# Kernel tuning notes

Measured on AMD Instinct MI355X. Metric: run time of the kernel, lower is better.

## Reference

```python
import jax, jax.numpy as jnp
import numpy as np

B, S, D, UNITS = 64, 2048, 1024, 1024


def setup_inputs() -> dict:
    key = jax.random.key(0)
    ks = jax.random.split(key, 5)
    sc = 1.0 / np.sqrt(D)
    return {
        "s_prev": jax.random.normal(ks[0], (B, D), jnp.float32),
        "hidden_states": jax.random.normal(ks[1], (B, S, D), jnp.float32),
        "W_kernel": jax.random.normal(ks[2], (D, UNITS), jnp.float32) * sc,
        "W_bias": jnp.zeros((UNITS,), jnp.float32),
        "U_kernel": jax.random.normal(ks[3], (D, UNITS), jnp.float32) * sc,
        "U_bias": jnp.zeros((UNITS,), jnp.float32),
        "V_kernel": jax.random.normal(ks[4], (UNITS, 1), jnp.float32) * (1.0 / np.sqrt(UNITS)),
        "V_bias": jnp.zeros((1,), jnp.float32),
    }


def reference(s_prev, hidden_states, W_kernel, W_bias, U_kernel, U_bias, V_kernel, V_bias):
    # W(s_prev): [B, units], broadcast over seq axis
    w_s = (s_prev @ W_kernel + W_bias)[:, None, :]          # [B, 1, units]
    u_h = jnp.einsum('bsd,du->bsu', hidden_states, U_kernel) + U_bias  # [B, S, units]
    scores = jnp.tanh(w_s + u_h) @ V_kernel + V_bias        # [B, S, 1]
    weight = jax.nn.softmax(scores, axis=1)                 # [B, S, 1]
    context = jnp.sum(hidden_states * weight, axis=1)       # [B, D]
    return (context, weight)
```

## Files before the change

kernel.cpp:

```cpp
#include <hip/hip_runtime.h>
#include <stdint.h>

#define NB 64
#define NS 2048
#define ND 1024
#define NU 1024

typedef __attribute__((ext_vector_type(8))) _Float16 f16x8;
typedef __attribute__((ext_vector_type(4))) float f32x4;

__device__ __forceinline__ void gload_lds16(const void* g, void* l) {
    __builtin_amdgcn_global_load_lds(
        (const __attribute__((address_space(1))) unsigned int*)g,
        (__attribute__((address_space(3))) unsigned int*)l, 16, 0, 0);
}

__global__ void transpose_u(const float* __restrict__ Uk, _Float16* __restrict__ Ut) {
    __shared__ float tile[64][65];
    int d0 = blockIdx.x * 64, u0 = blockIdx.y * 64;
    int tid = threadIdx.x;
    #pragma unroll
    for (int i = 0; i < 16; ++i) {
        int idx = i * 256 + tid;
        int r = idx >> 6, c = idx & 63;
        tile[r][c] = Uk[(size_t)(d0 + r) * NU + (u0 + c)];
    }
    __syncthreads();
    #pragma unroll
    for (int i = 0; i < 16; ++i) {
        int idx = i * 256 + tid;
        int c = idx >> 6, r = idx & 63;
        Ut[(size_t)(u0 + c) * ND + (d0 + r)] = (_Float16)tile[r][c];
    }
}

__global__ void prep_off(const float* __restrict__ s_prev, const float* __restrict__ Wk,
                         const float* __restrict__ Wb, const float* __restrict__ Ub,
                         float* __restrict__ off) {
    int blk = blockIdx.x;
    int b = blk >> 2, ut = blk & 3;
    int tid = threadIdx.x;
    int u = ut * 256 + tid;
    __shared__ float sp[ND];
    #pragma unroll
    for (int i = tid; i < ND; i += 256) sp[i] = s_prev[(size_t)b * ND + i];
    __syncthreads();
    float acc = 0.f;
    #pragma unroll 8
    for (int d = 0; d < ND; ++d) acc += sp[d] * Wk[(size_t)d * NU + u];
    off[(size_t)b * NU + u] = acc + Wb[u] + Ub[u];
}

__launch_bounds__(256, 2)
__global__ void scores_kernel(const float* __restrict__ h,
                              const _Float16* __restrict__ Ut,
                              const float* __restrict__ off,
                              const float* __restrict__ V,
                              float* __restrict__ scores)
{
    int hw = blockIdx.x;
    int chunk = gridDim.x >> 3;
    int logical = (hw & 7) * chunk + (hw >> 3);
    int ublk = logical & 7;
    int t2 = logical >> 3;
    int sblk = t2 & 15;
    int b = t2 >> 4;
    int s0 = sblk * 128, u0 = ublk * 128;

    __shared__ _Float16 As[128][32];
    __shared__ _Float16 Bs[128][32];

    int tid = threadIdx.x;
    int w = tid >> 6, l = tid & 63;
    int wr = w >> 1, wc = w & 1;
    int rg = l >> 4, cl = l & 15;

    f32x4 acc[4][4] = {};

    const float* hA = h + ((size_t)b * NS + s0) * ND;

    const _Float16* srcB[2];
    #pragma unroll
    for (int i = 0; i < 2; ++i) {
        int row = w * 32 + i * 16 + (l >> 2);
        srcB[i] = Ut + (size_t)(u0 + row) * ND + (((l & 3) ^ ((row >> 1) & 3)) * 8);
    }

    int arow = tid >> 3;
    int aslog = (tid & 7) >> 1;
    int ahalf = tid & 1;

    float4 av0[4], av1[4];

    #define LOADA(dst, KK) { \
        int k0_ = (KK) * 32;  \
        _Pragma("unroll") \
        for (int p = 0; p < 4; ++p) \
            dst[p] = *(const float4*)(hA + (size_t)(p * 32 + arow) * ND + k0_ + (tid & 7) * 4); \
    }

    #define CVTW(src) { \
        _Pragma("unroll") \
        for (int p = 0; p < 4; ++p) { \
            int r_ = p * 32 + arow; \
            int sp_ = aslog ^ ((r_ >> 1) & 3); \
            union { _Float16 e[4]; uint2 u2; } cv; \
            cv.e[0] = (_Float16)src[p].x; cv.e[1] = (_Float16)src[p].y; \
            cv.e[2] = (_Float16)src[p].z; cv.e[3] = (_Float16)src[p].w; \
            *(uint2*)&As[r_][sp_ * 8 + ahalf * 4] = cv.u2; \
        } \
    }

    #define COMPUTE(KK) { \
        f16x8 af[4], bf[4]; \
        _Pragma("unroll") \
        for (int m = 0; m < 4; ++m) { \
            int r_ = wr * 64 + m * 16 + cl; \
            af[m] = *(const f16x8*)&As[r_][(rg ^ ((r_ >> 1) & 3)) * 8]; \
        } \
        _Pragma("unroll") \
        for (int n = 0; n < 4; ++n) { \
            int r_ = wc * 64 + n * 16 + cl; \
            bf[n] = *(const f16x8*)&Bs[r_][(rg ^ ((r_ >> 1) & 3)) * 8]; \
        } \
        _Pragma("unroll") \
        for (int m = 0; m < 4; ++m) \
            _Pragma("unroll") \
            for (int n = 0; n < 4; ++n) \
                acc[m][n] = __builtin_amdgcn_mfma_f32_16x16x32_f16(af[m], bf[n], acc[m][n], 0, 0, 0); \
    }

    #define ISSUEB(KK) { \
        _Pragma("unroll") \
        for (int i = 0; i < 2; ++i) \
            gload_lds16((const void*)(srcB[i] + (KK) * 32), (void*)&Bs[w * 32 + i * 16][0]); \
    }

    LOADA(av0, 0);
    for (int kk = 0; kk < 32; kk += 2) {
        __syncthreads();
        ISSUEB(kk);
        CVTW(av0);
        LOADA(av1, kk + 1);
        __syncthreads();
        COMPUTE(kk);

        __syncthreads();
        ISSUEB(kk + 1);
        CVTW(av1);
        if (kk + 2 < 32) LOADA(av0, kk + 2);
        __syncthreads();
        COMPUTE(kk + 1);
    }

    float offv[4], vv[4];
    #pragma unroll
    for (int n = 0; n < 4; ++n) {
        int u = u0 + wc * 64 + n * 16 + cl;
        offv[n] = off[(size_t)b * NU + u];
        vv[n] = V[u];
    }
    #pragma unroll
    for (int m = 0; m < 4; ++m) {
        #pragma unroll
        for (int i = 0; i < 4; ++i) {
            float sacc = 0.f;
            #pragma unroll
            for (int n = 0; n < 4; ++n) {
                float x = acc[m][n][i] + offv[n];
                float t = 1.0f - 2.0f / (1.0f + __expf(2.0f * x));
                sacc += t * vv[n];
            }
            #pragma unroll
            for (int msk = 1; msk < 16; msk <<= 1) sacc += __shfl_xor(sacc, msk, 64);
            if (cl == 0)
                atomicAdd(&scores[(size_t)b * NS + s0 + wr * 64 + m * 16 + rg * 4 + i], sacc);
        }
    }
    #undef LOADA
    #undef CVTW
    #undef COMPUTE
    #undef ISSUEB
}

__global__ void softmax_kernel(const float* __restrict__ scores, float* __restrict__ outw) {
    int b = blockIdx.x, tid = threadIdx.x;
    const float* src = scores + (size_t)b * NS;
    float4 x0 = *(const float4*)(src + tid * 8);
    float4 x1 = *(const float4*)(src + tid * 8 + 4);
    float m = fmaxf(fmaxf(fmaxf(x0.x, x0.y), fmaxf(x0.z, x0.w)),
                    fmaxf(fmaxf(x1.x, x1.y), fmaxf(x1.z, x1.w)));
    #pragma unroll
    for (int msk = 1; msk < 64; msk <<= 1) m = fmaxf(m, __shfl_xor(m, msk, 64));
    __shared__ float redm[4], reds[4];
    if ((tid & 63) == 0) redm[tid >> 6] = m;
    __syncthreads();
    m = fmaxf(fmaxf(redm[0], redm[1]), fmaxf(redm[2], redm[3]));
    float e[8];
    e[0] = __expf(x0.x - m); e[1] = __expf(x0.y - m); e[2] = __expf(x0.z - m); e[3] = __expf(x0.w - m);
    e[4] = __expf(x1.x - m); e[5] = __expf(x1.y - m); e[6] = __expf(x1.z - m); e[7] = __expf(x1.w - m);
    float s = e[0] + e[1] + e[2] + e[3] + e[4] + e[5] + e[6] + e[7];
    #pragma unroll
    for (int msk = 1; msk < 64; msk <<= 1) s += __shfl_xor(s, msk, 64);
    if ((tid & 63) == 0) reds[tid >> 6] = s;
    __syncthreads();
    float Z = reds[0] + reds[1] + reds[2] + reds[3];
    float r = 1.0f / Z;
    float4 o0 = { e[0] * r, e[1] * r, e[2] * r, e[3] * r };
    float4 o1 = { e[4] * r, e[5] * r, e[6] * r, e[7] * r };
    *(float4*)(outw + (size_t)b * NS + tid * 8) = o0;
    *(float4*)(outw + (size_t)b * NS + tid * 8 + 4) = o1;
}

__global__ void context_partial(const float* __restrict__ h, const float* __restrict__ wgt,
                                float* __restrict__ part) {
    int sc = blockIdx.x, b = blockIdx.y, tid = threadIdx.x;
    __shared__ float lw[128];
    if (tid < 128) lw[tid] = wgt[(size_t)b * NS + sc * 128 + tid];
    __syncthreads();
    const float* hb = h + ((size_t)b * NS + sc * 128) * ND + tid * 4;
    float4 acc = { 0.f, 0.f, 0.f, 0.f };
    #pragma unroll 4
    for (int s = 0; s < 128; ++s) {
        float4 hv = *(const float4*)(hb + (size_t)s * ND);
        float wv = lw[s];
        acc.x += hv.x * wv; acc.y += hv.y * wv; acc.z += hv.z * wv; acc.w += hv.w * wv;
    }
    *(float4*)(part + ((size_t)(sc * NB + b)) * ND + tid * 4) = acc;
}

__global__ void context_reduce(const float* __restrict__ part, float* __restrict__ outc) {
    int b = blockIdx.x, tid = threadIdx.x;
    float4 acc = { 0.f, 0.f, 0.f, 0.f };
    #pragma unroll
    for (int k = 0; k < 16; ++k) {
        float4 p = *(const float4*)(part + ((size_t)(k * NB + b)) * ND + tid * 4);
        acc.x += p.x; acc.y += p.y; acc.z += p.z; acc.w += p.w;
    }
    *(float4*)(outc + (size_t)b * ND + tid * 4) = acc;
}

extern "C" void kernel_launch(void* const* d_in, const int* in_sizes, int n_in,
                              void* d_out, int out_size, void* d_ws, size_t ws_size,
                              hipStream_t stream) {
    const float* s_prev = (const float*)d_in[0];
    const float* hidden = (const float*)d_in[1];
    const float* Wk     = (const float*)d_in[2];
    const float* Wb     = (const float*)d_in[3];
    const float* Uk     = (const float*)d_in[4];
    const float* Ub     = (const float*)d_in[5];
    const float* Vk     = (const float*)d_in[6];

    float* out_ctx = (float*)d_out;
    float* out_w   = out_ctx + NB * ND;

    char* ws = (char*)d_ws;
    _Float16* Ut  = (_Float16*)ws;
    float* off    = (float*)(ws + (size_t)(2 << 20));
    float* scores = (float*)(ws + (size_t)(2 << 20) + (256 << 10));
    float* part   = (float*)(ws + (size_t)(2 << 20) + (768 << 10));

    hipMemsetAsync(scores, 0, (size_t)NB * NS * sizeof(float), stream);
    transpose_u<<<dim3(16, 16), 256, 0, stream>>>(Uk, Ut);
    prep_off<<<256, 256, 0, stream>>>(s_prev, Wk, Wb, Ub, off);
    scores_kernel<<<8192, 256, 0, stream>>>(hidden, Ut, off, Vk, scores);
    softmax_kernel<<<NB, 256, 0, stream>>>(scores, out_w);
    context_partial<<<dim3(16, NB), 256, 0, stream>>>(hidden, out_w, part);
    context_reduce<<<NB, 256, 0, stream>>>(part, out_ctx);
}
```

Measured before the change: 646.0 us.

## Stream fp32 A tiles directly to LDS and double-buffer the GEMM main loop

The A operand (hidden states) now goes from global memory straight into LDS as fp32 via global_load_lds with an XOR swizzle, and is converted to fp16 at fragment-load time instead of being staged through registers. Both A and B tiles are double-buffered, so the next k-slice is issued before computing the current one and each step needs one barrier instead of four. This is meant to cut register pressure and synchronisation and to overlap loads with MFMA work. In exchange, LDS use roughly triples (32 KB A plus 16 KB B per block), which may limit occupancy, and every wave repeats the fp32-to-fp16 conversion on each LDS read.

```diff
diff --git a/kernel.cpp b/kernel.cpp
--- a/kernel.cpp
+++ b/kernel.cpp
@@ -67,8 +67,8 @@
     int b = t2 >> 4;
     int s0 = sblk * 128, u0 = ublk * 128;
 
-    __shared__ _Float16 As[128][32];
-    __shared__ _Float16 Bs[128][32];
+    __shared__ float As32[2][128][32];
+    __shared__ _Float16 Bs[2][128][32];
 
     int tid = threadIdx.x;
     int w = tid >> 6, l = tid & 63;
@@ -79,6 +79,13 @@
 
     const float* hA = h + ((size_t)b * NS + s0) * ND;
 
+    const float* srcA[4];
+    #pragma unroll
+    for (int i = 0; i < 4; ++i) {
+        int row = w * 32 + i * 8 + (l >> 3);
+        int gslot = (l & 7) ^ (row & 7);
+        srcA[i] = hA + (size_t)row * ND + gslot * 4;
+    }
     const _Float16* srcB[2];
     #pragma unroll
     for (int i = 0; i < 2; ++i) {
@@ -86,42 +93,36 @@
         srcB[i] = Ut + (size_t)(u0 + row) * ND + (((l & 3) ^ ((row >> 1) & 3)) * 8);
     }
 
-    int arow = tid >> 3;
-    int aslog = (tid & 7) >> 1;
-    int ahalf = tid & 1;
-
-    float4 av0[4], av1[4];
-
-    #define LOADA(dst, KK) { \
-        int k0_ = (KK) * 32;  \
-        _Pragma("unroll") \
-        for (int p = 0; p < 4; ++p) \
-            dst[p] = *(const float4*)(hA + (size_t)(p * 32 + arow) * ND + k0_ + (tid & 7) * 4); \
-    }
-
-    #define CVTW(src) { \
-        _Pragma("unroll") \
-        for (int p = 0; p < 4; ++p) { \
-            int r_ = p * 32 + arow; \
-            int sp_ = aslog ^ ((r_ >> 1) & 3); \
-            union { _Float16 e[4]; uint2 u2; } cv; \
-            cv.e[0] = (_Float16)src[p].x; cv.e[1] = (_Float16)src[p].y; \
-            cv.e[2] = (_Float16)src[p].z; cv.e[3] = (_Float16)src[p].w; \
-            *(uint2*)&As[r_][sp_ * 8 + ahalf * 4] = cv.u2; \
-        } \
-    }
-
-    #define COMPUTE(KK) { \
+    #define STAGE(BUF, KK) { \
+        _Pragma("unroll") \
+        for (int i = 0; i < 4; ++i) \
+            gload_lds16((const void*)(srcA[i] + (KK) * 32), (void*)&As32[BUF][w * 32 + i * 8][0]); \
+        _Pragma("unroll") \
+        for (int i = 0; i < 2; ++i) \
+            gload_lds16((const void*)(srcB[i] + (KK) * 32), (void*)&Bs[BUF][w * 32 + i * 16][0]); \
+    }
+
+    #define COMPUTE(BUF) { \
         f16x8 af[4], bf[4]; \
         _Pragma("unroll") \
         for (int m = 0; m < 4; ++m) { \
             int r_ = wr * 64 + m * 16 + cl; \
-            af[m] = *(const f16x8*)&As[r_][(rg ^ ((r_ >> 1) & 3)) * 8]; \
+            int msk_ = r_ & 7; \
+            int p0 = (((rg << 1) ^ msk_)) * 4; \
+            int p1 = ((((rg << 1) | 1) ^ msk_)) * 4; \
+            f32x4 lo = *(const f32x4*)&As32[BUF][r_][p0]; \
+            f32x4 hi = *(const f32x4*)&As32[BUF][r_][p1]; \
+            f16x8 a; \
+            a[0] = (_Float16)lo[0]; a[1] = (_Float16)lo[1]; \
+            a[2] = (_Float16)lo[2]; a[3] = (_Float16)lo[3]; \
+            a[4] = (_Float16)hi[0]; a[5] = (_Float16)hi[1]; \
+            a[6] = (_Float16)hi[2]; a[7] = (_Float16)hi[3]; \
+            af[m] = a; \
         } \
         _Pragma("unroll") \
         for (int n = 0; n < 4; ++n) { \
             int r_ = wc * 64 + n * 16 + cl; \
-            bf[n] = *(const f16x8*)&Bs[r_][(rg ^ ((r_ >> 1) & 3)) * 8]; \
+            bf[n] = *(const f16x8*)&Bs[BUF][r_][(rg ^ ((r_ >> 1) & 3)) * 8]; \
         } \
         _Pragma("unroll") \
         for (int m = 0; m < 4; ++m) \
@@ -130,28 +131,18 @@
                 acc[m][n] = __builtin_amdgcn_mfma_f32_16x16x32_f16(af[m], bf[n], acc[m][n], 0, 0, 0); \
     }
 
-    #define ISSUEB(KK) { \
-        _Pragma("unroll") \
-        for (int i = 0; i < 2; ++i) \
-            gload_lds16((const void*)(srcB[i] + (KK) * 32), (void*)&Bs[w * 32 + i * 16][0]); \
-    }
-
-    LOADA(av0, 0);
-    for (int kk = 0; kk < 32; kk += 2) {
+    STAGE(0, 0);
+    __syncthreads();
+
+    for (int kk = 0; kk < 31; ++kk) {
+        STAGE((kk + 1) & 1, kk + 1);
+        COMPUTE(kk & 1);
         __syncthreads();
-        ISSUEB(kk);
-        CVTW(av0);
-        LOADA(av1, kk + 1);
-        __syncthreads();
-        COMPUTE(kk);
-
-        __syncthreads();
-        ISSUEB(kk + 1);
-        CVTW(av1);
-        if (kk + 2 < 32) LOADA(av0, kk + 2);
-        __syncthreads();
-        COMPUTE(kk + 1);
-    }
+    }
+    COMPUTE(1);
+
+    #undef STAGE
+    #undef COMPUTE
 
     float offv[4], vv[4];
     #pragma unroll
@@ -177,10 +168,6 @@
                 atomicAdd(&scores[(size_t)b * NS + s0 + wr * 64 + m * 16 + rg * 4 + i], sacc);
         }
     }
-    #undef LOADA
-    #undef CVTW
-    #undef COMPUTE
-    #undef ISSUEB
 }
 
 __global__ void softmax_kernel(const float* __restrict__ scores, float* __restrict__ outw) {
```

Measured after the change: 773.9 us. 19.8% more time.

## Multi-buffer LDS tiles with one barrier per k-step and raise occupancy

Applied to the files above, without the earlier changes.

Moves the scores GEMM main loop from single LDS buffers with four barriers per two k-steps to double-buffered A and triple-buffered B tiles. Each k-step now needs only one barrier, and explicit vmcnt/lgkmcnt waits let global loads overlap compute. Launch bounds go from 2 to 4 blocks per CU, which caps registers per thread and may cause spills. The hand-tuned waitcnt counts depend on the exact order of issued loads, so a later change to that order could silently break correctness.

```diff
diff --git a/kernel.cpp b/kernel.cpp
--- a/kernel.cpp
+++ b/kernel.cpp
@@ -51,7 +51,7 @@
     off[(size_t)b * NU + u] = acc + Wb[u] + Ub[u];
 }
 
-__launch_bounds__(256, 2)
+__launch_bounds__(256, 4)
 __global__ void scores_kernel(const float* __restrict__ h,
                               const _Float16* __restrict__ Ut,
                               const float* __restrict__ off,
@@ -67,8 +67,8 @@
     int b = t2 >> 4;
     int s0 = sblk * 128, u0 = ublk * 128;
 
-    __shared__ _Float16 As[128][32];
-    __shared__ _Float16 Bs[128][32];
+    __shared__ _Float16 As[2][128][32];
+    __shared__ _Float16 Bs[3][128][32];
 
     int tid = threadIdx.x;
     int w = tid >> 6, l = tid & 63;
@@ -79,6 +79,10 @@
 
     const float* hA = h + ((size_t)b * NS + s0) * ND;
 
+    int arow = tid >> 3;
+    int acol4 = (tid & 7) * 4;
+    int aslog = (tid & 7) >> 1;
+    int ahalf = tid & 1;
     const _Float16* srcB[2];
     #pragma unroll
     for (int i = 0; i < 2; ++i) {
@@ -86,42 +90,43 @@
         srcB[i] = Ut + (size_t)(u0 + row) * ND + (((l & 3) ^ ((row >> 1) & 3)) * 8);
     }
 
-    int arow = tid >> 3;
-    int aslog = (tid & 7) >> 1;
-    int ahalf = tid & 1;
-
-    float4 av0[4], av1[4];
-
-    #define LOADA(dst, KK) { \
-        int k0_ = (KK) * 32;  \
+    float4 av[4];
+
+    #define LOADA(KK) { \
         _Pragma("unroll") \
         for (int p = 0; p < 4; ++p) \
-            dst[p] = *(const float4*)(hA + (size_t)(p * 32 + arow) * ND + k0_ + (tid & 7) * 4); \
-    }
-
-    #define CVTW(src) { \
+            av[p] = *(const float4*)(hA + (size_t)(p * 32 + arow) * ND + (KK) * 32 + acol4); \
+    }
+
+    #define ISSUEB(BI, KK) { \
+        _Pragma("unroll") \
+        for (int i = 0; i < 2; ++i) \
+            gload_lds16((const void*)(srcB[i] + (KK) * 32), (void*)&Bs[BI][w * 32 + i * 16][0]); \
+    }
+
+    #define CVTW(ABUF) { \
         _Pragma("unroll") \
         for (int p = 0; p < 4; ++p) { \
             int r_ = p * 32 + arow; \
             int sp_ = aslog ^ ((r_ >> 1) & 3); \
             union { _Float16 e[4]; uint2 u2; } cv; \
-            cv.e[0] = (_Float16)src[p].x; cv.e[1] = (_Float16)src[p].y; \
-            cv.e[2] = (_Float16)src[p].z; cv.e[3] = (_Float16)src[p].w; \
-            *(uint2*)&As[r_][sp_ * 8 + ahalf * 4] = cv.u2; \
+            cv.e[0] = (_Float16)av[p].x; cv.e[1] = (_Float16)av[p].y; \
+            cv.e[2] = (_Float16)av[p].z; cv.e[3] = (_Float16)av[p].w; \
+            *(uint2*)&As[ABUF][r_][sp_ * 8 + ahalf * 4] = cv.u2; \
         } \
     }
 
-    #define COMPUTE(KK) { \
+    #define COMPUTE(ABUF, BI) { \
         f16x8 af[4], bf[4]; \
         _Pragma("unroll") \
         for (int m = 0; m < 4; ++m) { \
             int r_ = wr * 64 + m * 16 + cl; \
-            af[m] = *(const f16x8*)&As[r_][(rg ^ ((r_ >> 1) & 3)) * 8]; \
+            af[m] = *(const f16x8*)&As[ABUF][r_][(rg ^ ((r_ >> 1) & 3)) * 8]; \
         } \
         _Pragma("unroll") \
         for (int n = 0; n < 4; ++n) { \
             int r_ = wc * 64 + n * 16 + cl; \
-            bf[n] = *(const f16x8*)&Bs[r_][(rg ^ ((r_ >> 1) & 3)) * 8]; \
+            bf[n] = *(const f16x8*)&Bs[BI][r_][(rg ^ ((r_ >> 1) & 3)) * 8]; \
         } \
         _Pragma("unroll") \
         for (int m = 0; m < 4; ++m) \
@@ -130,28 +135,37 @@
                 acc[m][n] = __builtin_amdgcn_mfma_f32_16x16x32_f16(af[m], bf[n], acc[m][n], 0, 0, 0); \
     }
 
-    #define ISSUEB(KK) { \
-        _Pragma("unroll") \
-        for (int i = 0; i < 2; ++i) \
-            gload_lds16((const void*)(srcB[i] + (KK) * 32), (void*)&Bs[w * 32 + i * 16][0]); \
-    }
-
-    LOADA(av0, 0);
-    for (int kk = 0; kk < 32; kk += 2) {
-        __syncthreads();
-        ISSUEB(kk);
-        CVTW(av0);
-        LOADA(av1, kk + 1);
-        __syncthreads();
-        COMPUTE(kk);
-
-        __syncthreads();
-        ISSUEB(kk + 1);
-        CVTW(av1);
-        if (kk + 2 < 32) LOADA(av0, kk + 2);
-        __syncthreads();
-        COMPUTE(kk + 1);
-    }
+    LOADA(0);
+    ISSUEB(0, 0);
+
+    int bcur = 0;
+    for (int t = 0; t < 31; ++t) {
+        asm volatile("s_waitcnt vmcnt(2)" ::: "memory");
+        __builtin_amdgcn_sched_barrier(0);
+        CVTW(t & 1);
+        LOADA(t + 1);
+        int bnxt = bcur + 1; if (bnxt == 3) bnxt = 0;
+        ISSUEB(bnxt, t + 1);
+        asm volatile("s_waitcnt vmcnt(6) lgkmcnt(0)" ::: "memory");
+        __builtin_amdgcn_sched_barrier(0);
+        __builtin_amdgcn_s_barrier();
+        __builtin_amdgcn_sched_barrier(0);
+        COMPUTE(t & 1, bcur);
+        bcur = bnxt;
+    }
+    asm volatile("s_waitcnt vmcnt(0)" ::: "memory");
+    __builtin_amdgcn_sched_barrier(0);
+    CVTW(1);
+    asm volatile("s_waitcnt lgkmcnt(0)" ::: "memory");
+    __builtin_amdgcn_sched_barrier(0);
+    __builtin_amdgcn_s_barrier();
+    __builtin_amdgcn_sched_barrier(0);
+    COMPUTE(1, bcur);
+
+    #undef LOADA
+    #undef ISSUEB
+    #undef CVTW
+    #undef COMPUTE
 
     float offv[4], vv[4];
     #pragma unroll
@@ -177,10 +191,6 @@
                 atomicAdd(&scores[(size_t)b * NS + s0 + wr * 64 + m * 16 + rg * 4 + i], sacc);
         }
     }
-    #undef LOADA
-    #undef CVTW
-    #undef COMPUTE
-    #undef ISSUEB
 }
 
 __global__ void softmax_kernel(const float* __restrict__ scores, float* __restrict__ outw) {
```

Measured after the change: 578.1 us. 1.12x faster.
